# Kernel optimization log

Hardware: AMD Instinct MI355X
Metric: run time of the kernel (lower is better)

The kernel has to match this reference:

```python
import jax, jax.numpy as jnp
import numpy as np

N = 50000      # nodes
E = 800000     # edges (avg degree 16)
F_IN = 128
HID = 64
NCLS = 40
K = 2          # num_stacks
T = 2          # num_layers (shared weights)


def setup_inputs() -> dict:
    key = jax.random.key(0)
    ks = jax.random.split(key, 10)
    s = 0.05
    return {
        "x": jax.random.normal(ks[0], (N, F_IN), dtype=jnp.float32),
        "edge_index": jax.random.randint(ks[1], (2, E), 0, N),
        "w1_init": jax.random.normal(ks[2], (K, F_IN, HID), dtype=jnp.float32) * s,
        "w1": jax.random.normal(ks[3], (K, HID, HID), dtype=jnp.float32) * s,
        "v1": jax.random.normal(ks[4], (K, F_IN, HID), dtype=jnp.float32) * s,
        "b1": jax.random.normal(ks[5], (K, HID), dtype=jnp.float32) * s,
        "w2_init": jax.random.normal(ks[6], (K, HID, NCLS), dtype=jnp.float32) * s,
        "w2": jax.random.normal(ks[7], (K, NCLS, NCLS), dtype=jnp.float32) * s,
        "v2": jax.random.normal(ks[8], (K, HID, NCLS), dtype=jnp.float32) * s,
        "b2": jax.random.normal(ks[9], (K, NCLS), dtype=jnp.float32) * s,
    }


def _gcn_norm(src, dst, n):
    # PyG gcn_norm with add_self_loops=False: deg over destination, sym norm
    deg = jax.ops.segment_sum(jnp.ones_like(dst, dtype=jnp.float32), dst, num_segments=n)
    dinv = jnp.where(deg > 0, 1.0 / jnp.sqrt(deg), 0.0)
    return dinv[src] * dinv[dst]  # [E]


def _arma_conv(x, src, dst, norm, n, w_init, w, v, b, act):
    # x: [N, Fin]; w_init: [K, Fin, Fout]; w: [K, Fout, Fout]; v: [K, Fin, Fout]; b: [K, Fout]
    root = jnp.einsum('nf,kfg->kng', x, v)  # [K, N, Fout], dropout=0 -> identity
    out = None
    for t in range(T):
        if t == 0:
            h = jnp.einsum('nf,kfg->kng', x, w_init)
        else:
            h = jnp.einsum('knf,kfg->kng', out, w)
        # sparse neighbor aggregation: out[i] = sum_{(j->i)} norm_e * h[j]
        agg = jax.vmap(
            lambda hk: jax.ops.segment_sum(hk[src] * norm[:, None], dst, num_segments=n)
        )(h)  # [K, N, Fout]
        out = act(agg + root + b[:, None, :])
    return out.mean(axis=0)  # mean over stacks -> [N, Fout]


def reference(x, edge_index, w1_init, w1, v1, b1, w2_init, w2, v2, b2):
    src, dst = edge_index[0], edge_index[1]
    norm = _gcn_norm(src, dst, N)
    h = _arma_conv(x, src, dst, norm, N, w1_init, w1, v1, b1, jax.nn.relu)
    h = jax.nn.relu(h)  # wrapper ReLU; dropout is identity in eval
    o = _arma_conv(h, src, dst, norm, N, w2_init, w2, v2, b2, lambda z: z)
    return jax.nn.log_softmax(o, axis=1)
```

## Files before the change

### kernel.cpp

```cpp
#include <hip/hip_runtime.h>
#include <hip/hip_bf16.h>
#include <math.h>

#define N_NODES 50000
#define F_IN 128
#define HID 64
#define NCLS 40
#define K_STACKS 2
#define SCAN_TILE 1024
#define NBLK_CNT 256

typedef __attribute__((ext_vector_type(8))) short short8;
typedef __attribute__((ext_vector_type(4))) float floatx4;
typedef __attribute__((ext_vector_type(2))) float floatx2;

__device__ __forceinline__ unsigned int f32_to_bf16_bits(float f) {
    unsigned int u = __float_as_uint(f);
    return (u + 0x7fffu + ((u >> 16) & 1u)) >> 16;
}
__device__ __forceinline__ unsigned int pack_bf16x2(float a, float b) {
    return f32_to_bf16_bits(a) | (f32_to_bf16_bits(b) << 16);
}
__device__ __forceinline__ unsigned char f32_to_fp8(float v) {
    int pk = __builtin_amdgcn_cvt_pk_fp8_f32(v, v, 0, false);
    return (unsigned char)(pk & 0xff);
}


__global__ __launch_bounds__(256) void count_kernel(const int* __restrict__ dst,
                                                    int* __restrict__ counts, int E) {
    __shared__ int hist[256];
    int blk = blockIdx.x, t = threadIdx.x;
    hist[t] = 0;
    __syncthreads();
    int chunk = (E + NBLK_CNT - 1) / NBLK_CNT;
    int s = blk * chunk, e = min(E, s + chunk);
    for (int i = s + t; i < e; i += 256) atomicAdd(&hist[dst[i] >> 8], 1);
    __syncthreads();
    counts[t * NBLK_CNT + blk] = hist[t];
}

__global__ __launch_bounds__(256) void scan_phase1(const int* __restrict__ in,
                                                   int* __restrict__ blockSums, int n) {
    __shared__ int lds[256];
    int b = blockIdx.x, t = threadIdx.x;
    int base = b * SCAN_TILE + t * 4;
    int s = 0;
    if (base + 3 < n) {
        int4 v = *(const int4*)(in + base);
        s = v.x + v.y + v.z + v.w;
    } else {
#pragma unroll
        for (int i = 0; i < 4; ++i)
            if (base + i < n) s += in[base + i];
    }
    lds[t] = s;
    __syncthreads();
    for (int off = 128; off; off >>= 1) {
        if (t < off) lds[t] += lds[t + off];
        __syncthreads();
    }
    if (t == 0) blockSums[b] = lds[0];
}

__global__ void scan_phase2(int* __restrict__ blockSums, int nb) {
    int t = threadIdx.x;
    int v = (t < nb) ? blockSums[t] : 0;
#pragma unroll
    for (int off = 1; off < 64; off <<= 1) {
        int u = __shfl_up(v, off);
        if (t >= off) v += u;
    }
    if (t < nb) blockSums[t] = v;
}

__global__ __launch_bounds__(256) void scan_phase3_excl(const int* __restrict__ in,
                                                        const int* __restrict__ blockSumsInc,
                                                        int* __restrict__ out, int n) {
    __shared__ int lds[256];
    int b = blockIdx.x, t = threadIdx.x;
    int base = b * SCAN_TILE + t * 4;
    int e[4];
    int s = 0;
#pragma unroll
    for (int i = 0; i < 4; ++i) {
        e[i] = (base + i < n) ? in[base + i] : 0;
        s += e[i];
    }
    lds[t] = s;
    __syncthreads();
    int v = s;
    for (int off = 1; off < 256; off <<= 1) {
        int add = (t >= off) ? lds[t - off] : 0;
        __syncthreads();
        v += add;
        lds[t] = v;
        __syncthreads();
    }
    int run = (t == 0 ? 0 : lds[t - 1]) + (b == 0 ? 0 : blockSumsInc[b - 1]);
#pragma unroll
    for (int i = 0; i < 4; ++i) {
        if (base + i < n) {
            out[base + i] = run;
            run += e[i];
        }
    }
}

__global__ __launch_bounds__(256) void bucket_scatter_kernel(const int* __restrict__ src,
                                                             const int* __restrict__ dst,
                                                             const int* __restrict__ scanned,
                                                             unsigned int* __restrict__ pairs,
                                                             int E) {
    __shared__ int cur[256];
    int blk = blockIdx.x, t = threadIdx.x;
    cur[t] = scanned[t * NBLK_CNT + blk];
    __syncthreads();
    int chunk = (E + NBLK_CNT - 1) / NBLK_CNT;
    int s0 = blk * chunk, e0 = min(E, s0 + chunk);
    for (int i = s0 + t; i < e0; i += 256) {
        int d = dst[i];
        int pos = atomicAdd(&cur[d >> 8], 1);
        pairs[pos] = (unsigned int)src[i] | ((unsigned int)(d & 255) << 16);
    }
}

__global__ __launch_bounds__(256) void csr_build_kernel(const unsigned int* __restrict__ pairs,
                                                        const int* __restrict__ scanned,
                                                        int* __restrict__ row_ptr,
                                                        float* __restrict__ dinv,
                                                        int* __restrict__ col, int N, int E) {
    __shared__ int degl[256], lds[256], curl[256], sb[2];
    int b = blockIdx.x, t = threadIdx.x;
    if (t == 0) {
        sb[0] = scanned[b * NBLK_CNT];
        sb[1] = (b + 1 < 256) ? scanned[(b + 1) * NBLK_CNT] : E;
    }
    degl[t] = 0;
    __syncthreads();
    int bstart = sb[0], bend = sb[1];
    for (int e = bstart + t; e < bend; e += 256) {
        atomicAdd(&degl[(pairs[e] >> 16) & 255], 1);
    }
    __syncthreads();
    int d = degl[t];
    lds[t] = d;
    __syncthreads();
    int v = d;
    for (int off = 1; off < 256; off <<= 1) {
        int add = (t >= off) ? lds[t - off] : 0;
        __syncthreads();
        v += add;
        lds[t] = v;
        __syncthreads();
    }
    int excl = v - d;
    int node = b * 256 + t;
    if (node <= N) row_ptr[node] = bstart + excl;
    if (node < N) dinv[node] = (d > 0) ? (1.0f / sqrtf((float)d)) : 0.0f;
    curl[t] = excl;
    __syncthreads();
    for (int e = bstart + t; e < bend; e += 256) {
        unsigned int p = pairs[e];
        int ln = (p >> 16) & 255;
        int pos = atomicAdd(&curl[ln], 1);
        col[bstart + pos] = (int)(p & 0xffffu);
    }
}

__device__ __forceinline__ void wt_one(const float* __restrict__ in,
                                       unsigned short* __restrict__ out, int li, int C, int F,
                                       int CP) {
    int k = li / (F * CP);
    int r = li - k * F * CP;
    int f = r / CP;
    int c = r - f * CP;
    out[li] = (c < C) ? (unsigned short)f32_to_bf16_bits(in[((size_t)k * C + c) * F + f]) : 0;
}

__global__ void wt_all_kernel(const float* v1, const float* w1i, const float* w1,
                              const float* v2, const float* w2i, const float* w2,
                              unsigned short* v1t, unsigned short* w1it, unsigned short* w1t,
                              unsigned short* v2t, unsigned short* w2it, unsigned short* w2t) {
    int i = blockIdx.x * blockDim.x + threadIdx.x;
    if (i < 16384) wt_one(v1, v1t, i, 128, 64, 128);
    else if (i < 32768) wt_one(w1i, w1it, i - 16384, 128, 64, 128);
    else if (i < 40960) wt_one(w1, w1t, i - 32768, 64, 64, 64);
    else if (i < 46080) wt_one(v2, v2t, i - 40960, 64, 40, 64);
    else if (i < 51200) wt_one(w2i, w2it, i - 46080, 64, 40, 64);
    else if (i < 56320) wt_one(w2, w2t, i - 51200, 40, 40, 64);
}

template <int CINP>
__device__ __forceinline__ void stage_A(const void* A, unsigned short* At, size_t abase,
                                        int n0, int t, int N, int CREAL, int a_bf16) {
    constexpr int CP8 = CINP / 8;
    constexpr int MS = CP8 - 1;
    constexpr int SH = (CP8 == 16) ? 4 : 3;
    for (int i = t; i < 64 * CP8; i += 256) {
        int n = i >> SH;
        int c = i & MS;
        uint4 w = make_uint4(0u, 0u, 0u, 0u);
        int gn = n0 + n;
        if (gn < N && c * 8 < CREAL) {
            if (a_bf16) {
                w = *(const uint4*)((const unsigned short*)A + abase + (size_t)gn * CREAL + c * 8);
            } else {
                const float* srcp = (const float*)A + abase + (size_t)gn * CREAL + c * 8;
                float4 f0 = *(const float4*)(srcp);
                float4 f1 = *(const float4*)(srcp + 4);
                w.x = pack_bf16x2(f0.x, f0.y);
                w.y = pack_bf16x2(f0.z, f0.w);
                w.z = pack_bf16x2(f1.x, f1.y);
                w.w = pack_bf16x2(f1.z, f1.w);
            }
        }
        *(uint4*)(At + n * CINP + ((c ^ (n & MS)) << 3)) = w;
    }
}

template <int CINP>
__device__ __forceinline__ void stage_B(const unsigned short* Bk, unsigned short* Bs, int t,
                                        int COUT) {
    constexpr int CP8 = CINP / 8;
    constexpr int MS = CP8 - 1;
    constexpr int SH = (CP8 == 16) ? 4 : 3;
    for (int i = t; i < COUT * CP8; i += 256) {
        int f = i >> SH;
        int c = i & MS;
        uint4 w = *(const uint4*)(Bk + f * CINP + c * 8);
        *(uint4*)(Bs + f * CINP + ((c ^ (f & MS)) << 3)) = w;
    }
}

template <int CINP>
__global__ __launch_bounds__(256) void gemm_mfma(
    const void* __restrict__ A, const unsigned short* __restrict__ Bt,
    void* __restrict__ out, const float* __restrict__ scale, int N, int COUT, int CREAL,
    int a_per_k, int a_bf16, int out_fp8, int do_scale, int out_inter) {
    constexpr int CP8 = CINP / 8;
    constexpr int MS = CP8 - 1;
    __shared__ __align__(16) unsigned short At[64 * CINP];
    __shared__ __align__(16) unsigned short Bs[64 * CINP];

    const int k = blockIdx.y;
    const int n0 = blockIdx.x * 64;
    const int t = threadIdx.x;
    stage_A<CINP>(A, At, a_per_k ? (size_t)k * N * CREAL : (size_t)0, n0, t, N, CREAL, a_bf16);
    stage_B<CINP>(Bt + (size_t)k * COUT * CINP, Bs, t, COUT);
    __syncthreads();

    const int lane = t & 63;
    const int wv = t >> 6;
    const int quad = lane >> 4;
    const int li = lane & 15;
    const int m0 = wv * 16;

    floatx4 acc[4] = {{0.f, 0.f, 0.f, 0.f}, {0.f, 0.f, 0.f, 0.f},
                      {0.f, 0.f, 0.f, 0.f}, {0.f, 0.f, 0.f, 0.f}};
    const int am = (m0 + li) & MS;
#pragma unroll
    for (int kc = 0; kc < CINP / 32; ++kc) {
        int cc = kc * 4 + quad;
        short8 a = *(const short8*)(At + (m0 + li) * CINP + ((cc ^ am) << 3));
#pragma unroll
        for (int nt = 0; nt < 4; ++nt) {
            if (nt * 16 < COUT) {
                int f = nt * 16 + li;
                short8 b = *(const short8*)(Bs + f * CINP + ((cc ^ (f & MS)) << 3));
                acc[nt] = __builtin_amdgcn_mfma_f32_16x16x32_bf16(a, b, acc[nt], 0, 0, 0);
            }
        }
    }

    float sc[4] = {1.f, 1.f, 1.f, 1.f};
    if (do_scale) {
#pragma unroll
        for (int r = 0; r < 4; ++r) {
            int node = n0 + m0 + quad * 4 + r;
            sc[r] = (node < N) ? scale[node] : 1.f;
        }
    }
#pragma unroll
    for (int nt = 0; nt < 4; ++nt) {
        if (nt * 16 >= COUT) continue;
        int f = nt * 16 + li;
        if (f >= COUT) continue;
#pragma unroll
        for (int r = 0; r < 4; ++r) {
            int node = n0 + m0 + quad * 4 + r;
            if (node < N) {
                float val = acc[nt][r] * sc[r];
                if (out_inter) {
                    size_t o = (size_t)node * 2 * COUT + (size_t)k * COUT + f;
                    if (out_fp8)
                        ((unsigned char*)out)[o] = f32_to_fp8(val);
                    else
                        ((unsigned short*)out)[o] = (unsigned short)f32_to_bf16_bits(val);
                } else {
                    size_t o = ((size_t)k * N + node) * COUT + f;
                    ((float*)out)[o] = val;
                }
            }
        }
    }
}

template <int CINP>
__global__ __launch_bounds__(256) void gemm2_mfma(
    const void* __restrict__ A, const unsigned short* __restrict__ Bt1,
    const unsigned short* __restrict__ Bt2, unsigned short* __restrict__ out1,
    unsigned char* __restrict__ out2, const float* __restrict__ scale, int N, int COUT,
    int CREAL, int a_bf16) {
    constexpr int MS = CINP / 8 - 1;
    __shared__ __align__(16) unsigned short At[64 * CINP];
    __shared__ __align__(16) unsigned short Bs1[64 * CINP];
    __shared__ __align__(16) unsigned short Bs2[64 * CINP];

    const int k = blockIdx.y;
    const int n0 = blockIdx.x * 64;
    const int t = threadIdx.x;
    stage_A<CINP>(A, At, (size_t)0, n0, t, N, CREAL, a_bf16);
    stage_B<CINP>(Bt1 + (size_t)k * COUT * CINP, Bs1, t, COUT);
    stage_B<CINP>(Bt2 + (size_t)k * COUT * CINP, Bs2, t, COUT);
    __syncthreads();

    const int lane = t & 63;
    const int wv = t >> 6;
    const int quad = lane >> 4;
    const int li = lane & 15;
    const int m0 = wv * 16;

    floatx4 acc1[4] = {{0.f, 0.f, 0.f, 0.f}, {0.f, 0.f, 0.f, 0.f},
                       {0.f, 0.f, 0.f, 0.f}, {0.f, 0.f, 0.f, 0.f}};
    floatx4 acc2[4] = {{0.f, 0.f, 0.f, 0.f}, {0.f, 0.f, 0.f, 0.f},
                       {0.f, 0.f, 0.f, 0.f}, {0.f, 0.f, 0.f, 0.f}};
    const int am = (m0 + li) & MS;
#pragma unroll
    for (int kc = 0; kc < CINP / 32; ++kc) {
        int cc = kc * 4 + quad;
        short8 a = *(const short8*)(At + (m0 + li) * CINP + ((cc ^ am) << 3));
#pragma unroll
        for (int nt = 0; nt < 4; ++nt) {
            if (nt * 16 < COUT) {
                int f = nt * 16 + li;
                int bo = f * CINP + ((cc ^ (f & MS)) << 3);
                short8 b1 = *(const short8*)(Bs1 + bo);
                short8 b2 = *(const short8*)(Bs2 + bo);
                acc1[nt] = __builtin_amdgcn_mfma_f32_16x16x32_bf16(a, b1, acc1[nt], 0, 0, 0);
                acc2[nt] = __builtin_amdgcn_mfma_f32_16x16x32_bf16(a, b2, acc2[nt], 0, 0, 0);
            }
        }
    }

    float sc[4];
#pragma unroll
    for (int r = 0; r < 4; ++r) {
        int node = n0 + m0 + quad * 4 + r;
        sc[r] = (node < N) ? scale[node] : 1.f;
    }
#pragma unroll
    for (int nt = 0; nt < 4; ++nt) {
        if (nt * 16 >= COUT) continue;
        int f = nt * 16 + li;
        if (f >= COUT) continue;
#pragma unroll
        for (int r = 0; r < 4; ++r) {
            int node = n0 + m0 + quad * 4 + r;
            if (node < N) {
                out1[((size_t)k * N + node) * COUT + f] =
                    (unsigned short)f32_to_bf16_bits(acc1[nt][r]);
                out2[(size_t)node * 2 * COUT + (size_t)k * COUT + f] =
                    f32_to_fp8(acc2[nt][r] * sc[r]);
            }
        }
    }
}

template <int F>
__global__ __launch_bounds__(256) void agg_kernel(
    const unsigned char* __restrict__ h8, const int* __restrict__ row_ptr,
    const int* __restrict__ col, const float* __restrict__ dinv,
    const unsigned short* __restrict__ rootb, const float* __restrict__ bias,
    void* __restrict__ out, int N, int do_relu, int mode) {
    constexpr int FH = F / 8;
    constexpr int ROWB = 2 * F;
    int wid = (blockIdx.x * blockDim.x + threadIdx.x) >> 6;
    int lane = threadIdx.x & 63;
    int half = lane >> 5;
    int l32 = lane & 31;
    int node = wid * 2 + half;
    bool valid = node < N;
    int e0 = 0, deg = 0;
    float dv = 0.f;
    if (valid) {
        e0 = row_ptr[node];
        deg = row_ptr[node + 1] - e0;
        dv = dinv[node];
    }
    const int sub = l32 >> 4;
    const int fq = l32 & 15;
    const int kk = fq >> 3;
    const int fqq = fq & 7;
    const int fqc = (fqq < FH) ? fqq : (FH - 1);
    const int foff = kk * F + fqc * 8;

    float acc[8] = {};
    for (int w0 = 0; w0 < deg; w0 += 32) {
        int mye = w0 + l32;
        int c = (mye < deg) ? col[e0 + mye] : 0;
        int nch = min(deg - w0, 32);
        for (int base = 0; base < nch; base += 16) {
            uint2 v[8];
            float wj[8];
#pragma unroll
            for (int u = 0; u < 8; ++u) {
                int j = base + u * 2 + sub;
                int cj = __shfl(c, (half << 5) | (j & 31));
                bool ok = (j < nch);
                wj[u] = ok ? 1.f : 0.f;
                int cs = ok ? cj : 0;
                v[u] = *(const uint2*)(h8 + (size_t)cs * ROWB + foff);
            }
#pragma unroll
            for (int u = 0; u < 8; ++u) {
                floatx2 f0 = __builtin_amdgcn_cvt_pk_f32_fp8(v[u].x, false);
                floatx2 f1 = __builtin_amdgcn_cvt_pk_f32_fp8(v[u].x, true);
                floatx2 f2 = __builtin_amdgcn_cvt_pk_f32_fp8(v[u].y, false);
                floatx2 f3 = __builtin_amdgcn_cvt_pk_f32_fp8(v[u].y, true);
                acc[0] += wj[u] * f0.x;
                acc[1] += wj[u] * f0.y;
                acc[2] += wj[u] * f1.x;
                acc[3] += wj[u] * f1.y;
                acc[4] += wj[u] * f2.x;
                acc[5] += wj[u] * f2.y;
                acc[6] += wj[u] * f3.x;
                acc[7] += wj[u] * f3.y;
            }
        }
    }
#pragma unroll
    for (int i = 0; i < 8; ++i) acc[i] += __shfl_xor(acc[i], 16);

    size_t oc = ((size_t)kk * N + (valid ? node : 0)) * F + fqc * 8;
    uint4 rv = *(const uint4*)(rootb + oc);
    const float* bp = bias + kk * F + fqc * 8;
    float4 b0 = *(const float4*)(bp);
    float4 b1 = *(const float4*)(bp + 4);
    const unsigned int ru[4] = {rv.x, rv.y, rv.z, rv.w};
    float res[8];
#pragma unroll
    for (int q = 0; q < 4; ++q) {
        float rlo = __uint_as_float(ru[q] << 16);
        float rhi = __uint_as_float(ru[q] & 0xffff0000u);
        float blo = (q < 2) ? ((q == 0) ? b0.x : b0.z) : ((q == 2) ? b1.x : b1.z);
        float bhi = (q < 2) ? ((q == 0) ? b0.y : b0.w) : ((q == 2) ? b1.y : b1.w);
        res[2 * q] = acc[2 * q] * dv + rlo + blo;
        res[2 * q + 1] = acc[2 * q + 1] * dv + rhi + bhi;
    }
    if (do_relu) {
#pragma unroll
        for (int i = 0; i < 8; ++i) res[i] = fmaxf(res[i], 0.f);
    }
    if (mode == 0) {
        if (sub == 0 && fqq < FH && valid) {
            size_t o = ((size_t)kk * N + node) * F + fqq * 8;
            uint4 w;
            w.x = pack_bf16x2(res[0], res[1]);
            w.y = pack_bf16x2(res[2], res[3]);
            w.z = pack_bf16x2(res[4], res[5]);
            w.w = pack_bf16x2(res[6], res[7]);
            *(uint4*)((unsigned short*)out + o) = w;
        }
    } else {
        float mres[8];
#pragma unroll
        for (int i = 0; i < 8; ++i) mres[i] = 0.5f * (res[i] + __shfl_xor(res[i], 8));
        if (sub == 0 && kk == 0 && fqq < FH && valid) {
            size_t o = (size_t)node * F + fqq * 8;
            *(float4*)((float*)out + o) = make_float4(mres[0], mres[1], mres[2], mres[3]);
            *(float4*)((float*)out + o + 4) = make_float4(mres[4], mres[5], mres[6], mres[7]);
        }
    }
}

__global__ __launch_bounds__(256) void lsm_kernel(const float* __restrict__ g,
                                                  float* __restrict__ out, int N) {
    int wid = (blockIdx.x * blockDim.x + threadIdx.x) >> 6;
    int lane = threadIdx.x & 63;
    if (wid >= N) return;
    float v = (lane < NCLS) ? g[(size_t)wid * NCLS + lane] : -INFINITY;
    float m = v;
#pragma unroll
    for (int off = 32; off; off >>= 1) m = fmaxf(m, __shfl_xor(m, off));
    float ex = (lane < NCLS) ? expf(v - m) : 0.f;
    float s = ex;
#pragma unroll
    for (int off = 32; off; off >>= 1) s += __shfl_xor(s, off);
    float r = v - m - logf(s);
    if (lane < NCLS) out[(size_t)wid * NCLS + lane] = r;
}


static inline size_t align256(size_t x) { return (x + 255) & ~(size_t)255; }

extern "C" void kernel_launch(void* const* d_in, const int* in_sizes, int n_in,
                              void* d_out, int out_size, void* d_ws, size_t ws_size,
                              hipStream_t stream) {
    const float* x = (const float*)d_in[0];
    const int* ei = (const int*)d_in[1];
    const float* w1_init = (const float*)d_in[2];
    const float* w1 = (const float*)d_in[3];
    const float* v1 = (const float*)d_in[4];
    const float* b1 = (const float*)d_in[5];
    const float* w2_init = (const float*)d_in[6];
    const float* w2 = (const float*)d_in[7];
    const float* v2 = (const float*)d_in[8];
    const float* b2 = (const float*)d_in[9];

    const int N = in_sizes[0] / F_IN;
    const int E = in_sizes[1] / 2;
    const int* src = ei;
    const int* dst = ei + E;

    char* p = (char*)d_ws;
    auto take = [&](size_t bytes) {
        char* r = p;
        p += align256(bytes);
        return r;
    };
    float* dinv = (float*)take((size_t)N * 4);
    int* row_ptr = (int*)take((size_t)(N + 1) * 4);
    int* blockSums = (int*)take(256 * 4);
    int* counts = (int*)take((size_t)256 * NBLK_CNT * 4);
    int* scanned = (int*)take((size_t)256 * NBLK_CNT * 4);
    unsigned int* pairs = (unsigned int*)take((size_t)E * 4);
    int* col = (int*)take((size_t)E * 4);
    unsigned short* v1t = (unsigned short*)take((size_t)2 * 64 * 128 * 2);
    unsigned short* w1it = (unsigned short*)take((size_t)2 * 64 * 128 * 2);
    unsigned short* w1t = (unsigned short*)take((size_t)2 * 64 * 64 * 2);
    unsigned short* v2t = (unsigned short*)take((size_t)2 * 40 * 64 * 2);
    unsigned short* w2it = (unsigned short*)take((size_t)2 * 40 * 64 * 2);
    unsigned short* w2t = (unsigned short*)take((size_t)2 * 40 * 64 * 2);
    unsigned short* rootb = (unsigned short*)take((size_t)K_STACKS * N * HID * 2);
    unsigned char* hb8 = (unsigned char*)take((size_t)K_STACKS * N * HID);
    unsigned short* hc = (unsigned short*)take((size_t)K_STACKS * N * HID * 2);
    float* h1 = (float*)take((size_t)N * HID * 4);
    float* gmean = (float*)take((size_t)N * NCLS * 4);

    const int TB = 256;
    const int nCnt = 256 * NBLK_CNT;
    const int nScanBlocks = nCnt / SCAN_TILE;
    const int nBuckets = (N + 255) / 256;

    count_kernel<<<NBLK_CNT, 256, 0, stream>>>(dst, counts, E);
    scan_phase1<<<nScanBlocks, 256, 0, stream>>>(counts, blockSums, nCnt);
    scan_phase2<<<1, 64, 0, stream>>>(blockSums, nScanBlocks);
    scan_phase3_excl<<<nScanBlocks, 256, 0, stream>>>(counts, blockSums, scanned, nCnt);
    bucket_scatter_kernel<<<NBLK_CNT, 256, 0, stream>>>(src, dst, scanned, pairs, E);
    csr_build_kernel<<<nBuckets, 256, 0, stream>>>(pairs, scanned, row_ptr, dinv, col, N, E);

    wt_all_kernel<<<(56320 + TB - 1) / TB, TB, 0, stream>>>(v1, w1_init, w1, v2, w2_init, w2,
                                                            v1t, w1it, w1t, v2t, w2it, w2t);

    dim3 ggrid((N + 63) / 64, K_STACKS);
    const int agg_blocks = ((N + 1) / 2 + 3) / 4;

    gemm2_mfma<128><<<ggrid, 256, 0, stream>>>(x, v1t, w1it, rootb, hb8, dinv, N, HID, 128, 0);
    agg_kernel<HID><<<agg_blocks, 256, 0, stream>>>(hb8, row_ptr, col, dinv, rootb, b1, hc, N, 1, 0);
    gemm_mfma<64><<<ggrid, 256, 0, stream>>>(hc, w1t, hb8, dinv, N, HID, 64, 1, 1, 1, 1, 1);
    agg_kernel<HID><<<agg_blocks, 256, 0, stream>>>(hb8, row_ptr, col, dinv, rootb, b1, h1, N, 1, 1);

    gemm2_mfma<64><<<ggrid, 256, 0, stream>>>(h1, v2t, w2it, rootb, hb8, dinv, N, NCLS, 64, 0);
    agg_kernel<NCLS><<<agg_blocks, 256, 0, stream>>>(hb8, row_ptr, col, dinv, rootb, b2, hc, N, 0, 0);
    gemm_mfma<64><<<ggrid, 256, 0, stream>>>(hc, w2t, hb8, dinv, N, NCLS, 40, 1, 1, 1, 1, 1);
    agg_kernel<NCLS><<<agg_blocks, 256, 0, stream>>>(hb8, row_ptr, col, dinv, rootb, b2, gmean, N, 0, 1);

    lsm_kernel<<<(N + 3) / 4, 256, 0, stream>>>(gmean, (float*)d_out, N);
}
```

Measured before the change: 286.1 us.

## Fuse scan phases into count kernel, loop stacks in gemm2, fuse log-softmax into aggregation

Three unrelated changes. The count kernel now accumulates per-tile sums with atomics, so the separate scan_phase1 and scan_phase2 launches are dropped and phase3 computes tile offsets itself. gemm2_mfma loops over both stacks inside one block, so the A tile is staged once instead of once per stack. The final aggregation gains a mode that applies log-softmax in-register, removing the lsm kernel and the gmean round trip. Together these cut launch count and memory traffic, at the cost of halving gemm2 grid parallelism and adding a memset.

```diff
diff --git a/kernel.cpp b/kernel.cpp
--- a/kernel.cpp
+++ b/kernel.cpp
@@ -28,57 +28,31 @@
 
 
 __global__ __launch_bounds__(256) void count_kernel(const int* __restrict__ dst,
-                                                    int* __restrict__ counts, int E) {
+                                                    int* __restrict__ counts,
+                                                    int* __restrict__ tileSums, int E) {
     __shared__ int hist[256];
+    __shared__ int ts[64];
     int blk = blockIdx.x, t = threadIdx.x;
     hist[t] = 0;
+    if (t < 64) ts[t] = 0;
     __syncthreads();
     int chunk = (E + NBLK_CNT - 1) / NBLK_CNT;
     int s = blk * chunk, e = min(E, s + chunk);
     for (int i = s + t; i < e; i += 256) atomicAdd(&hist[dst[i] >> 8], 1);
     __syncthreads();
     counts[t * NBLK_CNT + blk] = hist[t];
-}
-
-__global__ __launch_bounds__(256) void scan_phase1(const int* __restrict__ in,
-                                                   int* __restrict__ blockSums, int n) {
-    __shared__ int lds[256];
-    int b = blockIdx.x, t = threadIdx.x;
-    int base = b * SCAN_TILE + t * 4;
-    int s = 0;
-    if (base + 3 < n) {
-        int4 v = *(const int4*)(in + base);
-        s = v.x + v.y + v.z + v.w;
-    } else {
-#pragma unroll
-        for (int i = 0; i < 4; ++i)
-            if (base + i < n) s += in[base + i];
-    }
-    lds[t] = s;
-    __syncthreads();
-    for (int off = 128; off; off >>= 1) {
-        if (t < off) lds[t] += lds[t + off];
-        __syncthreads();
-    }
-    if (t == 0) blockSums[b] = lds[0];
-}
-
-__global__ void scan_phase2(int* __restrict__ blockSums, int nb) {
-    int t = threadIdx.x;
-    int v = (t < nb) ? blockSums[t] : 0;
-#pragma unroll
-    for (int off = 1; off < 64; off <<= 1) {
-        int u = __shfl_up(v, off);
-        if (t >= off) v += u;
-    }
-    if (t < nb) blockSums[t] = v;
+    atomicAdd(&ts[t >> 2], hist[t]);
+    __syncthreads();
+    if (t < 64) atomicAdd(&tileSums[t], ts[t]);
 }
 
 __global__ __launch_bounds__(256) void scan_phase3_excl(const int* __restrict__ in,
-                                                        const int* __restrict__ blockSumsInc,
+                                                        const int* __restrict__ tileSums,
                                                         int* __restrict__ out, int n) {
     __shared__ int lds[256];
+    __shared__ int tsum[64];
     int b = blockIdx.x, t = threadIdx.x;
+    if (t < 64) tsum[t] = tileSums[t];
     int base = b * SCAN_TILE + t * 4;
     int e[4];
     int s = 0;
@@ -97,7 +71,9 @@
         lds[t] = v;
         __syncthreads();
     }
-    int run = (t == 0 ? 0 : lds[t - 1]) + (b == 0 ? 0 : blockSumsInc[b - 1]);
+    int toff = 0;
+    for (int i = 0; i < b; ++i) toff += tsum[i];
+    int run = (t == 0 ? 0 : lds[t - 1]) + toff;
 #pragma unroll
     for (int i = 0; i < 4; ++i) {
         if (base + i < n) {
@@ -238,8 +214,7 @@
     const void* __restrict__ A, const unsigned short* __restrict__ Bt,
     void* __restrict__ out, const float* __restrict__ scale, int N, int COUT, int CREAL,
     int a_per_k, int a_bf16, int out_fp8, int do_scale, int out_inter) {
-    constexpr int CP8 = CINP / 8;
-    constexpr int MS = CP8 - 1;
+    constexpr int MS = CINP / 8 - 1;
     __shared__ __align__(16) unsigned short At[64 * CINP];
     __shared__ __align__(16) unsigned short Bs[64 * CINP];
 
@@ -317,41 +292,16 @@
     __shared__ __align__(16) unsigned short Bs1[64 * CINP];
     __shared__ __align__(16) unsigned short Bs2[64 * CINP];
 
-    const int k = blockIdx.y;
     const int n0 = blockIdx.x * 64;
     const int t = threadIdx.x;
     stage_A<CINP>(A, At, (size_t)0, n0, t, N, CREAL, a_bf16);
-    stage_B<CINP>(Bt1 + (size_t)k * COUT * CINP, Bs1, t, COUT);
-    stage_B<CINP>(Bt2 + (size_t)k * COUT * CINP, Bs2, t, COUT);
-    __syncthreads();
 
     const int lane = t & 63;
     const int wv = t >> 6;
     const int quad = lane >> 4;
     const int li = lane & 15;
     const int m0 = wv * 16;
-
-    floatx4 acc1[4] = {{0.f, 0.f, 0.f, 0.f}, {0.f, 0.f, 0.f, 0.f},
-                       {0.f, 0.f, 0.f, 0.f}, {0.f, 0.f, 0.f, 0.f}};
-    floatx4 acc2[4] = {{0.f, 0.f, 0.f, 0.f}, {0.f, 0.f, 0.f, 0.f},
-                       {0.f, 0.f, 0.f, 0.f}, {0.f, 0.f, 0.f, 0.f}};
     const int am = (m0 + li) & MS;
-#pragma unroll
-    for (int kc = 0; kc < CINP / 32; ++kc) {
-        int cc = kc * 4 + quad;
-        short8 a = *(const short8*)(At + (m0 + li) * CINP + ((cc ^ am) << 3));
-#pragma unroll
-        for (int nt = 0; nt < 4; ++nt) {
-            if (nt * 16 < COUT) {
-                int f = nt * 16 + li;
-                int bo = f * CINP + ((cc ^ (f & MS)) << 3);
-                short8 b1 = *(const short8*)(Bs1 + bo);
-                short8 b2 = *(const short8*)(Bs2 + bo);
-                acc1[nt] = __builtin_amdgcn_mfma_f32_16x16x32_bf16(a, b1, acc1[nt], 0, 0, 0);
-                acc2[nt] = __builtin_amdgcn_mfma_f32_16x16x32_bf16(a, b2, acc2[nt], 0, 0, 0);
-            }
-        }
-    }
 
     float sc[4];
 #pragma unroll
@@ -359,19 +309,47 @@
         int node = n0 + m0 + quad * 4 + r;
         sc[r] = (node < N) ? scale[node] : 1.f;
     }
-#pragma unroll
-    for (int nt = 0; nt < 4; ++nt) {
-        if (nt * 16 >= COUT) continue;
-        int f = nt * 16 + li;
-        if (f >= COUT) continue;
-#pragma unroll
-        for (int r = 0; r < 4; ++r) {
-            int node = n0 + m0 + quad * 4 + r;
-            if (node < N) {
-                out1[((size_t)k * N + node) * COUT + f] =
-                    (unsigned short)f32_to_bf16_bits(acc1[nt][r]);
-                out2[(size_t)node * 2 * COUT + (size_t)k * COUT + f] =
-                    f32_to_fp8(acc2[nt][r] * sc[r]);
+
+    for (int k = 0; k < 2; ++k) {
+        if (k) __syncthreads();
+        stage_B<CINP>(Bt1 + (size_t)k * COUT * CINP, Bs1, t, COUT);
+        stage_B<CINP>(Bt2 + (size_t)k * COUT * CINP, Bs2, t, COUT);
+        __syncthreads();
+
+        floatx4 acc1[4] = {{0.f, 0.f, 0.f, 0.f}, {0.f, 0.f, 0.f, 0.f},
+                           {0.f, 0.f, 0.f, 0.f}, {0.f, 0.f, 0.f, 0.f}};
+        floatx4 acc2[4] = {{0.f, 0.f, 0.f, 0.f}, {0.f, 0.f, 0.f, 0.f},
+                           {0.f, 0.f, 0.f, 0.f}, {0.f, 0.f, 0.f, 0.f}};
+#pragma unroll
+        for (int kc = 0; kc < CINP / 32; ++kc) {
+            int cc = kc * 4 + quad;
+            short8 a = *(const short8*)(At + (m0 + li) * CINP + ((cc ^ am) << 3));
+#pragma unroll
+            for (int nt = 0; nt < 4; ++nt) {
+                if (nt * 16 < COUT) {
+                    int f = nt * 16 + li;
+                    int bo = f * CINP + ((cc ^ (f & MS)) << 3);
+                    short8 b1 = *(const short8*)(Bs1 + bo);
+                    short8 b2 = *(const short8*)(Bs2 + bo);
+                    acc1[nt] = __builtin_amdgcn_mfma_f32_16x16x32_bf16(a, b1, acc1[nt], 0, 0, 0);
+                    acc2[nt] = __builtin_amdgcn_mfma_f32_16x16x32_bf16(a, b2, acc2[nt], 0, 0, 0);
+                }
+            }
+        }
+#pragma unroll
+        for (int nt = 0; nt < 4; ++nt) {
+            if (nt * 16 >= COUT) continue;
+            int f = nt * 16 + li;
+            if (f >= COUT) continue;
+#pragma unroll
+            for (int r = 0; r < 4; ++r) {
+                int node = n0 + m0 + quad * 4 + r;
+                if (node < N) {
+                    out1[((size_t)k * N + node) * COUT + f] =
+                        (unsigned short)f32_to_bf16_bits(acc1[nt][r]);
+                    out2[(size_t)node * 2 * COUT + (size_t)k * COUT + f] =
+                        f32_to_fp8(acc2[nt][r] * sc[r]);
+                }
             }
         }
     }
@@ -476,29 +454,38 @@
         float mres[8];
 #pragma unroll
         for (int i = 0; i < 8; ++i) mres[i] = 0.5f * (res[i] + __shfl_xor(res[i], 8));
-        if (sub == 0 && kk == 0 && fqq < FH && valid) {
-            size_t o = (size_t)node * F + fqq * 8;
-            *(float4*)((float*)out + o) = make_float4(mres[0], mres[1], mres[2], mres[3]);
-            *(float4*)((float*)out + o + 4) = make_float4(mres[4], mres[5], mres[6], mres[7]);
-        }
-    }
-}
-
-__global__ __launch_bounds__(256) void lsm_kernel(const float* __restrict__ g,
-                                                  float* __restrict__ out, int N) {
-    int wid = (blockIdx.x * blockDim.x + threadIdx.x) >> 6;
-    int lane = threadIdx.x & 63;
-    if (wid >= N) return;
-    float v = (lane < NCLS) ? g[(size_t)wid * NCLS + lane] : -INFINITY;
-    float m = v;
-#pragma unroll
-    for (int off = 32; off; off >>= 1) m = fmaxf(m, __shfl_xor(m, off));
-    float ex = (lane < NCLS) ? expf(v - m) : 0.f;
-    float s = ex;
-#pragma unroll
-    for (int off = 32; off; off >>= 1) s += __shfl_xor(s, off);
-    float r = v - m - logf(s);
-    if (lane < NCLS) out[(size_t)wid * NCLS + lane] = r;
+        if (mode == 1) {
+            if (sub == 0 && kk == 0 && fqq < FH && valid) {
+                size_t o = (size_t)node * F + fqq * 8;
+                *(float4*)((float*)out + o) = make_float4(mres[0], mres[1], mres[2], mres[3]);
+                *(float4*)((float*)out + o + 4) = make_float4(mres[4], mres[5], mres[6], mres[7]);
+            }
+        } else {
+            bool act = (fqq < FH);
+            float lm = -INFINITY;
+            if (act) {
+#pragma unroll
+                for (int i = 0; i < 8; ++i) lm = fmaxf(lm, mres[i]);
+            }
+#pragma unroll
+            for (int m = 1; m < 8; m <<= 1) lm = fmaxf(lm, __shfl_xor(lm, m));
+            float ls = 0.f;
+            if (act) {
+#pragma unroll
+                for (int i = 0; i < 8; ++i) ls += expf(mres[i] - lm);
+            }
+#pragma unroll
+            for (int m = 1; m < 8; m <<= 1) ls += __shfl_xor(ls, m);
+            float lg = lm + logf(ls);
+            if (sub == 0 && kk == 0 && act && valid) {
+                size_t o = (size_t)node * F + fqq * 8;
+                *(float4*)((float*)out + o) =
+                    make_float4(mres[0] - lg, mres[1] - lg, mres[2] - lg, mres[3] - lg);
+                *(float4*)((float*)out + o + 4) =
+                    make_float4(mres[4] - lg, mres[5] - lg, mres[6] - lg, mres[7] - lg);
+            }
+        }
+    }
 }
 
 
@@ -531,7 +518,7 @@
     };
     float* dinv = (float*)take((size_t)N * 4);
     int* row_ptr = (int*)take((size_t)(N + 1) * 4);
-    int* blockSums = (int*)take(256 * 4);
+    int* tileSums = (int*)take(256 * 4);
     int* counts = (int*)take((size_t)256 * NBLK_CNT * 4);
     int* scanned = (int*)take((size_t)256 * NBLK_CNT * 4);
     unsigned int* pairs = (unsigned int*)take((size_t)E * 4);
@@ -546,35 +533,33 @@
     unsigned char* hb8 = (unsigned char*)take((size_t)K_STACKS * N * HID);
     unsigned short* hc = (unsigned short*)take((size_t)K_STACKS * N * HID * 2);
     float* h1 = (float*)take((size_t)N * HID * 4);
-    float* gmean = (float*)take((size_t)N * NCLS * 4);
 
     const int TB = 256;
     const int nCnt = 256 * NBLK_CNT;
     const int nScanBlocks = nCnt / SCAN_TILE;
     const int nBuckets = (N + 255) / 256;
-
-    count_kernel<<<NBLK_CNT, 256, 0, stream>>>(dst, counts, E);
-    scan_phase1<<<nScanBlocks, 256, 0, stream>>>(counts, blockSums, nCnt);
-    scan_phase2<<<1, 64, 0, stream>>>(blockSums, nScanBlocks);
-    scan_phase3_excl<<<nScanBlocks, 256, 0, stream>>>(counts, blockSums, scanned, nCnt);
+    const int ntiles = (N + 63) / 64;
+
+    hipMemsetAsync(tileSums, 0, 256, stream);
+    count_kernel<<<NBLK_CNT, 256, 0, stream>>>(dst, counts, tileSums, E);
+    scan_phase3_excl<<<nScanBlocks, 256, 0, stream>>>(counts, tileSums, scanned, nCnt);
     bucket_scatter_kernel<<<NBLK_CNT, 256, 0, stream>>>(src, dst, scanned, pairs, E);
     csr_build_kernel<<<nBuckets, 256, 0, stream>>>(pairs, scanned, row_ptr, dinv, col, N, E);
 
     wt_all_kernel<<<(56320 + TB - 1) / TB, TB, 0, stream>>>(v1, w1_init, w1, v2, w2_init, w2,
                                                             v1t, w1it, w1t, v2t, w2it, w2t);
 
-    dim3 ggrid((N + 63) / 64, K_STACKS);
+    dim3 ggrid(ntiles, K_STACKS);
     const int agg_blocks = ((N + 1) / 2 + 3) / 4;
 
-    gemm2_mfma<128><<<ggrid, 256, 0, stream>>>(x, v1t, w1it, rootb, hb8, dinv, N, HID, 128, 0);
+    gemm2_mfma<128><<<ntiles, 256, 0, stream>>>(x, v1t, w1it, rootb, hb8, dinv, N, HID, 128, 0);
     agg_kernel<HID><<<agg_blocks, 256, 0, stream>>>(hb8, row_ptr, col, dinv, rootb, b1, hc, N, 1, 0);
     gemm_mfma<64><<<ggrid, 256, 0, stream>>>(hc, w1t, hb8, dinv, N, HID, 64, 1, 1, 1, 1, 1);
     agg_kernel<HID><<<agg_blocks, 256, 0, stream>>>(hb8, row_ptr, col, dinv, rootb, b1, h1, N, 1, 1);
 
-    gemm2_mfma<64><<<ggrid, 256, 0, stream>>>(h1, v2t, w2it, rootb, hb8, dinv, N, NCLS, 64, 0);
+    gemm2_mfma<64><<<ntiles, 256, 0, stream>>>(h1, v2t, w2it, rootb, hb8, dinv, N, NCLS, 64, 0);
     agg_kernel<NCLS><<<agg_blocks, 256, 0, stream>>>(hb8, row_ptr, col, dinv, rootb, b2, hc, N, 0, 0);
     gemm_mfma<64><<<ggrid, 256, 0, stream>>>(hc, w2t, hb8, dinv, N, NCLS, 40, 1, 1, 1, 1, 1);
-    agg_kernel<NCLS><<<agg_blocks, 256, 0, stream>>>(hb8, row_ptr, col, dinv, rootb, b2, gmean, N, 0, 1);
-
-    lsm_kernel<<<(N + 3) / 4, 256, 0, stream>>>(gmean, (float*)d_out, N);
-}
+    agg_kernel<NCLS><<<agg_blocks, 256, 0, stream>>>(hb8, row_ptr, col, dinv, rootb, b2,
+                                                     (float*)d_out, N, 0, 2);
+}
```

New measurement: 288.0 us. No clear change (+0.7%).
